# Kernel optimization log

Measured on AMD Instinct MI355X. Metric: run time of the kernel, lower is better.

The kernel has to match this reference:

```python
import jax, jax.numpy as jnp
import numpy as np

B, L, D, H, W, FF = 4, 4096, 1024, 16, 256, 4096
HD = D // H
EPS = 1e-6


def layernorm(x, gamma, beta):
    mean = x.mean(-1, keepdims=True)
    var = ((x - mean) ** 2).mean(-1, keepdims=True)  # unbiased=False
    return gamma * (x - mean) / jnp.sqrt(var + EPS) + beta


def setup_inputs() -> dict:
    key = jax.random.key(0)
    ks = jax.random.split(key, 6)
    s = 0.02
    return {
        "x": jax.random.normal(ks[0], (B, L, D), jnp.float32),
        "in_proj_w": jax.random.normal(ks[1], (3 * D, D), jnp.float32) * s,
        "in_proj_b": jnp.zeros((3 * D,), jnp.float32),
        "out_w": jax.random.normal(ks[2], (D, D), jnp.float32) * s,
        "out_b": jnp.zeros((D,), jnp.float32),
        "gamma1": jnp.ones((D,), jnp.float32),
        "beta1": jnp.zeros((D,), jnp.float32),
        "w1": jax.random.normal(ks[3], (D, FF), jnp.float32) * s,
        "bf1": jnp.zeros((FF,), jnp.float32),
        "w2": jax.random.normal(ks[4], (FF, D), jnp.float32) * s,
        "bf2": jnp.zeros((D,), jnp.float32),
        "gamma2": jnp.ones((D,), jnp.float32),
        "beta2": jnp.zeros((D,), jnp.float32),
    }


def reference(x, in_proj_w, in_proj_b, out_w, out_b, gamma1, beta1,
              w1, bf1, w2, bf2, gamma2, beta2):
    nC = L // W
    wq, wk, wv = jnp.split(in_proj_w, 3, axis=0)   # each [D, D], torch: y = x @ w.T + b
    bq, bk, bv = jnp.split(in_proj_b, 3)

    # chunk queries; kv window for chunk c = [chunk c-1, chunk c] (chunk 0: only itself)
    ch = x.reshape(B, nC, W, D)
    prev = jnp.concatenate([jnp.zeros_like(ch[:, :1]), ch[:, :-1]], axis=1)
    kv = jnp.concatenate([prev, ch], axis=2)       # [B, nC, 2W, D]

    q = (ch @ wq.T + bq).reshape(B, nC, W, H, HD)
    k = (kv @ wk.T + bk).reshape(B, nC, 2 * W, H, HD)
    v = (kv @ wv.T + bv).reshape(B, nC, 2 * W, H, HD)

    scores = jnp.einsum('bcqhd,bckhd->bchqk', q, k) / np.float32(np.sqrt(HD))
    # first W key slots of chunk 0 are padding -> mask them
    valid = (jnp.arange(2 * W)[None, :] >= W) | (jnp.arange(nC)[:, None] > 0)  # [nC, 2W]
    scores = jnp.where(valid[None, :, None, None, :], scores, jnp.float32(-1e9))
    attn = jax.nn.softmax(scores, axis=-1)

    o = jnp.einsum('bchqk,bckhd->bcqhd', attn, v).reshape(B, nC, W, D)
    attn_out = (o @ out_w.T + out_b).reshape(B, L, D)

    x1 = layernorm(x + attn_out, gamma1, beta1)
    ffn = jax.nn.relu(x1 @ w1 + bf1) @ w2 + bf2
    return layernorm(x1 + ffn, gamma2, beta2)
```

## Files before the change

kernel.cpp:

```cpp
#include <hip/hip_runtime.h>
#include <stdint.h>

#define Bsz 4
#define Lseq 4096
#define Dm 1024
#define Hh 16
#define Wc 256
#define FFd 4096
#define NC 16
#define NTOK (Bsz * Lseq)

typedef unsigned short u16;

__device__ __forceinline__ float bf2f(u16 u) {
  union { unsigned int i; float f; } v; v.i = ((unsigned int)u) << 16; return v.f;
}
__device__ __forceinline__ u16 f2bf(float f) {
  union { float f; unsigned int i; } v; v.f = f;
  unsigned int r = v.i + 0x7fffu + ((v.i >> 16) & 1u);
  return (u16)(r >> 16);
}
__device__ __forceinline__ unsigned int pack2bf(float a, float b) {
  union { float f; unsigned int u; } x, y; x.f = a; y.f = b;
  return ((x.u + 0x8000u) >> 16) | ((y.u + 0x8000u) & 0xffff0000u);
}

__global__ void cvt_f32_bf16(const float* __restrict__ in, u16* __restrict__ out, long n) {
  long i = ((long)blockIdx.x * blockDim.x + threadIdx.x) * 4;
  if (i >= n) return;
  float4 v = *(const float4*)(in + i);
  u16 o[4] = { f2bf(v.x), f2bf(v.y), f2bf(v.z), f2bf(v.w) };
  *(uint2*)(out + i) = *(const uint2*)o;
}

__global__ void transpose_f32_bf16(const float* __restrict__ in, u16* __restrict__ out,
                                   int R, int C) {
  __shared__ float tile[32][33];
  int tx = threadIdx.x & 31, ty = threadIdx.x >> 5;
  int r0 = blockIdx.y * 32, c0 = blockIdx.x * 32;
#pragma unroll
  for (int k = 0; k < 4; ++k)
    tile[ty + 8 * k][tx] = in[(size_t)(r0 + ty + 8 * k) * C + c0 + tx];
  __syncthreads();
#pragma unroll
  for (int k = 0; k < 4; ++k)
    out[(size_t)(c0 + ty + 8 * k) * R + r0 + tx] = f2bf(tile[tx][ty + 8 * k]);
}

typedef __attribute__((ext_vector_type(8))) short s16x8;
typedef __attribute__((ext_vector_type(4))) float fx4;
typedef __attribute__((address_space(1))) unsigned int as1u;
typedef __attribute__((address_space(3))) unsigned int as3u;
typedef __attribute__((address_space(3))) const u16 l16c;

__device__ __forceinline__ void gll16(const void* g, void* l) {
  __builtin_amdgcn_global_load_lds((as1u*)g, (as3u*)l, 16, 0, 0);
}

#define DSR(dst, base, IMM)                                                 \
  asm volatile("ds_read_b128 %0, %1 offset:" IMM : "=v"(dst) : "v"(base))

__device__ __forceinline__ void swizzle_mn(int MB, int NB, int* mb, int* nb) {
  int flat = blockIdx.y * NB + blockIdx.x;
  if ((MB & 7) == 0) {
    int xcd = flat & 7;
    int j = flat >> 3;
    int rpx = MB >> 3;
    *nb = j / rpx;
    int rowin = j - *nb * rpx;
    *mb = (rowin << 3) | xcd;
  } else {
    *mb = blockIdx.y; *nb = blockIdx.x;
  }
}

__device__ __forceinline__ void stage_seg(const u16* __restrict__ G, int ld, int k0,
                                          u16* L, int rb0, int rb1,
                                          int wid, int lane) {
#pragma unroll
  for (int i = 0; i < 2; ++i) {
    int j = wid * 2 + i;
    int rs = (j < 8) ? (rb0 + j * 8) : (rb1 + (j - 8) * 8);
    int grow = rs + (lane >> 3);
    int gcol = k0 + (((lane & 7) ^ (lane >> 3)) << 3);
    gll16(G + (size_t)grow * ld + gcol, L + rs * 64);
  }
}

#define MFMA_Q(MQ, NQ)                                                           \
  {                                                                              \
    _Pragma("unroll") for (int mt = 0; mt < 4; ++mt) {                           \
      _Pragma("unroll") for (int nt = 0; nt < 2; ++nt) {                         \
        acc[(MQ)*4 + mt][(NQ)*2 + nt] = __builtin_amdgcn_mfma_f32_16x16x32_bf16( \
            af[mt][0], bfr[NQ][nt][0], acc[(MQ)*4 + mt][(NQ)*2 + nt], 0, 0, 0);  \
        acc[(MQ)*4 + mt][(NQ)*2 + nt] = __builtin_amdgcn_mfma_f32_16x16x32_bf16( \
            af[mt][1], bfr[NQ][nt][1], acc[(MQ)*4 + mt][(NQ)*2 + nt], 0, 0, 0);  \
      }                                                                          \
    }                                                                            \
  }

#define WAIT_LGKM_FENCE()                                  \
  asm volatile("s_waitcnt lgkmcnt(0)" ::: "memory");       \
  __builtin_amdgcn_sched_barrier(0);

#define SB() __builtin_amdgcn_sched_barrier(0);

#define R_A_MQ0()                     \
  DSR(af[0][0], baseA0, "0");         \
  DSR(af[0][1], baseA1, "0");         \
  DSR(af[1][0], baseA0, "2048");      \
  DSR(af[1][1], baseA1, "2048");      \
  DSR(af[2][0], baseA0, "4096");      \
  DSR(af[2][1], baseA1, "4096");      \
  DSR(af[3][0], baseA0, "6144");      \
  DSR(af[3][1], baseA1, "6144");
#define R_A_MQ1()                     \
  DSR(af[0][0], baseA0, "8192");      \
  DSR(af[0][1], baseA1, "8192");      \
  DSR(af[1][0], baseA0, "10240");     \
  DSR(af[1][1], baseA1, "10240");     \
  DSR(af[2][0], baseA0, "12288");     \
  DSR(af[2][1], baseA1, "12288");     \
  DSR(af[3][0], baseA0, "14336");     \
  DSR(af[3][1], baseA1, "14336");
#define R_B_SEG0()                    \
  DSR(bfr[0][0][0], baseB0, "0");     \
  DSR(bfr[0][0][1], baseB1, "0");     \
  DSR(bfr[0][1][0], baseB0, "2048");  \
  DSR(bfr[0][1][1], baseB1, "2048");
#define R_B_SEG1()                    \
  DSR(bfr[1][0][0], baseB0, "4096");  \
  DSR(bfr[1][0][1], baseB1, "4096");  \
  DSR(bfr[1][1][0], baseB0, "6144");  \
  DSR(bfr[1][1][1], baseB1, "6144");

template <int RELU, int OUTBF16, int HASBIAS>
__global__ __launch_bounds__(512, 2) void gemm256(const u16* A, int lda,
                                                  const u16* Bm,
                                                  const float* __restrict__ bias,
                                                  void* Cp,
                                                  int M, int N, int K) {
  __shared__ __attribute__((aligned(16))) u16 As[2][256 * 64];
  __shared__ __attribute__((aligned(16))) u16 Bs[2][256 * 64];
  int tid = threadIdx.x;
  int lane = tid & 63, wid = tid >> 6;
  int lm = lane & 15, quad = lane >> 4;
  int wr = wid >> 2, wc = wid & 3;
  int mb, nb;
  swizzle_mn(gridDim.y, gridDim.x, &mb, &nb);
  int m0 = mb * 256, n0 = nb * 256;
  const u16* Ag = A + (size_t)m0 * lda;
  const u16* Bg = Bm + (size_t)n0 * K;
  int NT = K >> 6;

  int off0 = (quad ^ (lm & 7)) << 3;
  int off1 = ((4 + quad) ^ (lm & 7)) << 3;

  unsigned ldsA = (unsigned)(size_t)(l16c*)(&As[0][0]);
  unsigned ldsB = (unsigned)(size_t)(l16c*)(&Bs[0][0]);
  unsigned baseA0 = ldsA + (unsigned)(((wr * 128 + lm) * 64 + off0) * 2);
  unsigned baseA1 = ldsA + (unsigned)(((wr * 128 + lm) * 64 + off1) * 2);
  unsigned baseB0 = ldsB + (unsigned)(((wc * 64 + lm) * 64 + off0) * 2);
  unsigned baseB1 = ldsB + (unsigned)(((wc * 64 + lm) * 64 + off1) * 2);
  int sel = 32768;

  fx4 acc[8][4] = {};

  stage_seg(Ag, lda, 0, As[0], 0, 128, wid, lane);
  stage_seg(Ag, lda, 0, As[0], 64, 192, wid, lane);
  stage_seg(Bg, K, 0, Bs[0], 0, 64, wid, lane);
  stage_seg(Bg, K, 0, Bs[0], 128, 192, wid, lane);
  if (NT > 1) {
    stage_seg(Ag, lda, 64, As[1], 0, 128, wid, lane);
    stage_seg(Ag, lda, 64, As[1], 64, 192, wid, lane);
    asm volatile("s_waitcnt vmcnt(4)" ::: "memory");
  } else {
    asm volatile("s_waitcnt vmcnt(0)" ::: "memory");
  }
  __builtin_amdgcn_s_barrier();

  s16x8 af[4][2];
  s16x8 bfr[2][2][2];

  R_A_MQ0();
  R_B_SEG0();

  for (int t = 0; t < NT; ++t) {
    u16* Bn = Bs[(t + 1) & 1];
    u16* An2 = As[t & 1];
    int kn = (t + 1) << 6, kn2 = (t + 2) << 6;

    if (t + 1 < NT) stage_seg(Bg, K, kn, Bn, 0, 64, wid, lane);
    __builtin_amdgcn_s_barrier();
    WAIT_LGKM_FENCE()
    __builtin_amdgcn_s_setprio(1);
    MFMA_Q(0, 0)
    __builtin_amdgcn_s_setprio(0);
    SB()
    R_B_SEG1();
    __builtin_amdgcn_s_barrier();

    if (t + 1 < NT) stage_seg(Bg, K, kn, Bn, 128, 192, wid, lane);
    __builtin_amdgcn_s_barrier();
    WAIT_LGKM_FENCE()
    __builtin_amdgcn_s_setprio(1);
    MFMA_Q(0, 1)
    __builtin_amdgcn_s_setprio(0);
    SB()
    R_A_MQ1();
    __builtin_amdgcn_s_barrier();

    if (t + 2 < NT) stage_seg(Ag, lda, kn2, An2, 0, 128, wid, lane);
    __builtin_amdgcn_s_barrier();
    WAIT_LGKM_FENCE()
    __builtin_amdgcn_s_setprio(1);
    MFMA_Q(1, 1)
    __builtin_amdgcn_s_setprio(0);
    SB()
    __builtin_amdgcn_s_barrier();

    if (t + 2 < NT) {
      stage_seg(Ag, lda, kn2, An2, 64, 192, wid, lane);
      asm volatile("s_waitcnt vmcnt(4)" ::: "memory");
    } else if (t + 2 == NT) {
      asm volatile("s_waitcnt vmcnt(0)" ::: "memory");
    }
    __builtin_amdgcn_s_barrier();
    __builtin_amdgcn_s_setprio(1);
    MFMA_Q(1, 0)
    __builtin_amdgcn_s_setprio(0);
    SB()
    baseA0 += sel; baseA1 += sel; baseB0 += sel; baseB1 += sel; sel = -sel;
    if (t + 1 < NT) {
      R_A_MQ0();
      R_B_SEG0();
    }
    __builtin_amdgcn_s_barrier();
  }

  float* Cf = (float*)Cp;
  u16* Ch = (u16*)Cp;
#pragma unroll
  for (int ai = 0; ai < 8; ++ai) {
#pragma unroll
    for (int bi = 0; bi < 4; ++bi) {
      int col = n0 + wc * 64 + (bi >> 1) * 32 + (bi & 1) * 16 + lm;
      float bv = HASBIAS ? bias[col] : 0.f;
#pragma unroll
      for (int r = 0; r < 4; ++r) {
        int row = m0 + wr * 128 + (ai >> 2) * 64 + (ai & 3) * 16 + quad * 4 + r;
        float v = acc[ai][bi][r] + bv;
        if (RELU) v = v > 0.f ? v : 0.f;
        if (OUTBF16) Ch[(size_t)row * N + col] = f2bf(v);
        else         Cf[(size_t)row * N + col] = v;
      }
    }
  }
}

#define PADK 72
#define PADV 136
#define PADP 40
#define PADO 72

__global__ __launch_bounds__(256, 2) void attn_mfma(u16* qkv) {
  __shared__ __attribute__((aligned(16))) u16 lds[38400];
  u16* Klds  = lds;
  u16* Vtlds = lds + 9216;

  int bid = blockIdx.x;
  int h = bid & (Hh - 1);
  int c = (bid >> 4) & (NC - 1);
  int b = bid >> 8;
  int tid = threadIdx.x, lane = tid & 63, w = tid >> 6;
  int lm = lane & 15, quad = lane >> 4;
  u16* Pw = lds + 17920 + w * 5120;

  size_t rowbase = (size_t)b * Lseq;

  s16x8 qf[4][2];
#pragma unroll
  for (int nt = 0; nt < 4; ++nt)
#pragma unroll
    for (int ks = 0; ks < 2; ++ks) {
      int qtok = c * Wc + w * 64 + nt * 16 + lm;
      qf[nt][ks] = *(const s16x8*)(qkv + (rowbase + qtok) * 3072 + h * 64 + ks * 32 + quad * 8);
    }

  fx4 acc_o[4][4] = {};
  float lsum[4] = {0.f, 0.f, 0.f, 0.f};

  int nph = (c > 0) ? 4 : 2;
  int t0  = (c > 0) ? (c - 1) * Wc : 0;

  for (int ph = 0; ph < nph; ++ph) {
    int kt0 = t0 + ph * 128;
    __syncthreads();

#pragma unroll
    for (int it = 0; it < 4; ++it) {
      int s = tid + it * 256;
      int row = s >> 3, off = (s & 7) * 8;
      uint4 kv = *(const uint4*)(qkv + (rowbase + kt0 + row) * 3072 + 1024 + h * 64 + off);
      *(uint4*)(Klds + row * PADK + off) = kv;
    }
    {
      int d = lane;
      int kb = w * 32;
      u16 tmp[32];
#pragma unroll
      for (int i = 0; i < 32; ++i)
        tmp[i] = qkv[(rowbase + kt0 + kb + i) * 3072 + 2048 + h * 64 + d];
#pragma unroll
      for (int i = 0; i < 4; ++i)
        *(uint4*)(Vtlds + d * PADV + kb + i * 8) = *(const uint4*)(tmp + i * 8);
    }
    __syncthreads();

#pragma unroll
    for (int kt = 0; kt < 4; ++kt) {
      u16* Pb = Pw + (kt & 1) * 2560;
      fx4 sa[2][4] = {};
#pragma unroll
      for (int ks = 0; ks < 2; ++ks) {
        s16x8 kf0 = *(const s16x8*)(Klds + (kt * 32 + lm) * PADK + ks * 32 + quad * 8);
        s16x8 kf1 = *(const s16x8*)(Klds + (kt * 32 + 16 + lm) * PADK + ks * 32 + quad * 8);
#pragma unroll
        for (int nt = 0; nt < 4; ++nt) {
          sa[0][nt] = __builtin_amdgcn_mfma_f32_16x16x32_bf16(kf0, qf[nt][ks], sa[0][nt], 0, 0, 0);
          sa[1][nt] = __builtin_amdgcn_mfma_f32_16x16x32_bf16(kf1, qf[nt][ks], sa[1][nt], 0, 0, 0);
        }
      }
#pragma unroll
      for (int mt = 0; mt < 2; ++mt)
#pragma unroll
        for (int nt = 0; nt < 4; ++nt) {
          float e0 = __expf(sa[mt][nt][0] * 0.125f);
          float e1 = __expf(sa[mt][nt][1] * 0.125f);
          float e2 = __expf(sa[mt][nt][2] * 0.125f);
          float e3 = __expf(sa[mt][nt][3] * 0.125f);
          lsum[nt] += (e0 + e1) + (e2 + e3);
          uint2 pk; pk.x = pack2bf(e0, e1); pk.y = pack2bf(e2, e3);
          *(uint2*)(Pb + (nt * 16 + lm) * PADP + mt * 16 + quad * 4) = pk;
        }
#pragma unroll
      for (int mt = 0; mt < 4; ++mt) {
        s16x8 vf = *(const s16x8*)(Vtlds + (mt * 16 + lm) * PADV + kt * 32 + quad * 8);
#pragma unroll
        for (int nt = 0; nt < 4; ++nt) {
          s16x8 pf = *(const s16x8*)(Pb + (nt * 16 + lm) * PADP + quad * 8);
          acc_o[mt][nt] = __builtin_amdgcn_mfma_f32_16x16x32_bf16(vf, pf, acc_o[mt][nt], 0, 0, 0);
        }
      }
    }
  }

#pragma unroll
  for (int nt = 0; nt < 4; ++nt) {
    float v = lsum[nt];
    v += __shfl_xor(v, 16, 64);
    v += __shfl_xor(v, 32, 64);
    lsum[nt] = 1.f / v;
  }

  __syncthreads();
  u16* Obuf = lds;
#pragma unroll
  for (int mt = 0; mt < 4; ++mt)
#pragma unroll
    for (int nt = 0; nt < 4; ++nt) {
      float inv = lsum[nt];
      uint2 pk;
      pk.x = pack2bf(acc_o[mt][nt][0] * inv, acc_o[mt][nt][1] * inv);
      pk.y = pack2bf(acc_o[mt][nt][2] * inv, acc_o[mt][nt][3] * inv);
      int q = nt * 16 + lm;
      *(uint2*)(Obuf + (w * 64 + q) * PADO + mt * 16 + quad * 4) = pk;
    }
  __syncthreads();
#pragma unroll
  for (int it = 0; it < 8; ++it) {
    int s = tid + it * 256;
    int row = s >> 3, chunk = s & 7;
    uint4 v = *(const uint4*)(Obuf + row * PADO + chunk * 8);
    *(uint4*)(qkv + (rowbase + c * Wc + row) * 3072 + h * 64 + chunk * 8) = v;
  }
}

__device__ __forceinline__ void ln_core(float sx, float sy, float sz, float sw,
                                        const float* gamma, const float* beta, int tid,
                                        float* red, float4* outv) {
  float part = sx + sy + sz + sw;
#pragma unroll
  for (int off = 32; off > 0; off >>= 1) part += __shfl_down(part, off, 64);
  if ((tid & 63) == 0) red[tid >> 6] = part;
  __syncthreads();
  float mean = (red[0] + red[1] + red[2] + red[3]) * (1.f / 1024.f);
  __syncthreads();

  float dx = sx - mean, dy = sy - mean, dz = sz - mean, dw = sw - mean;
  float sq = dx * dx + dy * dy + dz * dz + dw * dw;
#pragma unroll
  for (int off = 32; off > 0; off >>= 1) sq += __shfl_down(sq, off, 64);
  if ((tid & 63) == 0) red[tid >> 6] = sq;
  __syncthreads();
  float var = (red[0] + red[1] + red[2] + red[3]) * (1.f / 1024.f);
  float rs = rsqrtf(var + 1e-6f);

  float4 g = *(const float4*)(gamma + tid * 4);
  float4 be = *(const float4*)(beta + tid * 4);
  outv->x = g.x * dx * rs + be.x;
  outv->y = g.y * dy * rs + be.y;
  outv->z = g.z * dz * rs + be.z;
  outv->w = g.w * dw * rs + be.w;
}

__global__ __launch_bounds__(256) void ln1_kernel(const float* __restrict__ r,
                                                  const float* __restrict__ dl,
                                                  const float* __restrict__ gamma,
                                                  const float* __restrict__ beta,
                                                  u16* __restrict__ outh) {
  __shared__ float red[4];
  int row = blockIdx.x, tid = threadIdx.x;
  size_t base = (size_t)row * Dm;
  float4 rv = *(const float4*)(r + base + tid * 4);
  float4 dv = *(const float4*)(dl + base + tid * 4);
  float4 o;
  ln_core(rv.x + dv.x, rv.y + dv.y, rv.z + dv.z, rv.w + dv.w, gamma, beta, tid, red, &o);
  u16 u[4] = { f2bf(o.x), f2bf(o.y), f2bf(o.z), f2bf(o.w) };
  *(uint2*)(outh + base + tid * 4) = *(const uint2*)u;
}

__global__ __launch_bounds__(256) void ln2_kernel(const u16* __restrict__ r,
                                                  const float* dl,
                                                  const float* __restrict__ colbias,
                                                  const float* __restrict__ gamma,
                                                  const float* __restrict__ beta,
                                                  float* outf) {
  __shared__ float red[4];
  int row = blockIdx.x, tid = threadIdx.x;
  size_t base = (size_t)row * Dm;
  uint2 ru = *(const uint2*)(r + base + tid * 4);
  const u16* pu = (const u16*)&ru;
  float4 dv = *(const float4*)(dl + base + tid * 4);
  float4 bb = *(const float4*)(colbias + tid * 4);
  float4 o;
  ln_core(bf2f(pu[0]) + dv.x + bb.x, bf2f(pu[1]) + dv.y + bb.y,
          bf2f(pu[2]) + dv.z + bb.z, bf2f(pu[3]) + dv.w + bb.w,
          gamma, beta, tid, red, &o);
  *(float4*)(outf + base + tid * 4) = o;
}

extern "C" void kernel_launch(void* const* d_in, const int* in_sizes, int n_in,
                              void* d_out, int out_size, void* d_ws, size_t ws_size,
                              hipStream_t stream) {
  const float* x         = (const float*)d_in[0];
  const float* in_proj_w = (const float*)d_in[1];
  const float* in_proj_b = (const float*)d_in[2];
  const float* out_w     = (const float*)d_in[3];
  const float* out_b     = (const float*)d_in[4];
  const float* gamma1    = (const float*)d_in[5];
  const float* beta1     = (const float*)d_in[6];
  const float* w1        = (const float*)d_in[7];
  const float* bf1       = (const float*)d_in[8];
  const float* w2        = (const float*)d_in[9];
  const float* bf2       = (const float*)d_in[10];
  const float* gamma2    = (const float*)d_in[11];
  const float* beta2     = (const float*)d_in[12];
  float* out = (float*)d_out;

  char* ws = (char*)d_ws;
  size_t off = 0;
  auto alloc = [&](size_t bytes) -> char* {
    char* p = ws + off;
    off += (bytes + 255) & ~(size_t)255;
    return p;
  };
  u16* wqkvh = (u16*)alloc((size_t)3 * Dm * Dm * 2);
  u16* owh   = (u16*)alloc((size_t)Dm * Dm * 2);
  u16* w1th  = (u16*)alloc((size_t)FFd * Dm * 2);
  u16* w2th  = (u16*)alloc((size_t)Dm * FFd * 2);
  u16* big   = (u16*)alloc((size_t)NTOK * FFd * 2);
  u16* x1h   = (u16*)alloc((size_t)NTOK * Dm * 2);
  u16* qkvh = big;
  u16* hh   = big;
  u16* xh   = (u16*)d_out;
  float* attnf = out;
  float* y2f   = out;

  cvt_f32_bf16<<<(long)NTOK * Dm / 1024, 256, 0, stream>>>(x, xh, (long)NTOK * Dm);
  cvt_f32_bf16<<<(long)3 * Dm * Dm / 1024, 256, 0, stream>>>(in_proj_w, wqkvh, (long)3 * Dm * Dm);
  cvt_f32_bf16<<<(long)Dm * Dm / 1024, 256, 0, stream>>>(out_w, owh, (long)Dm * Dm);
  transpose_f32_bf16<<<dim3(FFd / 32, Dm / 32), 256, 0, stream>>>(w1, w1th, Dm, FFd);
  transpose_f32_bf16<<<dim3(Dm / 32, FFd / 32), 256, 0, stream>>>(w2, w2th, FFd, Dm);

  gemm256<0, 1, 1><<<dim3(3 * Dm / 256, NTOK / 256), 512, 0, stream>>>(
      xh, Dm, wqkvh, in_proj_b, qkvh, NTOK, 3 * Dm, Dm);

  attn_mfma<<<Bsz * NC * Hh, 256, 0, stream>>>(qkvh);

  gemm256<0, 0, 1><<<dim3(Dm / 256, NTOK / 256), 512, 0, stream>>>(
      qkvh, 3 * Dm, owh, out_b, attnf, NTOK, Dm, Dm);

  ln1_kernel<<<NTOK, 256, 0, stream>>>(x, attnf, gamma1, beta1, x1h);

  gemm256<1, 1, 1><<<dim3(FFd / 256, NTOK / 256), 512, 0, stream>>>(
      x1h, Dm, w1th, bf1, hh, NTOK, FFd, Dm);

  gemm256<0, 0, 0><<<dim3(Dm / 256, NTOK / 256), 512, 0, stream>>>(
      hh, FFd, w2th, (const float*)nullptr, y2f, NTOK, Dm, FFd);

  ln2_kernel<<<NTOK, 256, 0, stream>>>(x1h, y2f, bf2, gamma2, beta2, out);
}
```

Baseline: 688.5 us.

## Pre-pack weights into MFMA fragment order and load B directly from global

Weights are repacked on device into an MFMA-fragment-ordered bf16 layout, so each wave can load its B operands straight from global memory into registers with dwordx4 loads, bypassing LDS. The freed LDS becomes a 4-stage ring buffer for the A tiles, and several barriers per K-step are removed. The goal is less LDS traffic and synchronisation, paid for with more global/L2 traffic on B (each wave fetches its own B fragments) and more register pressure from holding B in flight.

```diff
diff --git a/kernel.cpp b/kernel.cpp
--- a/kernel.cpp
+++ b/kernel.cpp
@@ -33,18 +33,44 @@
   *(uint2*)(out + i) = *(const uint2*)o;
 }
 
-__global__ void transpose_f32_bf16(const float* __restrict__ in, u16* __restrict__ out,
-                                   int R, int C) {
-  __shared__ float tile[32][33];
-  int tx = threadIdx.x & 31, ty = threadIdx.x >> 5;
-  int r0 = blockIdx.y * 32, c0 = blockIdx.x * 32;
-#pragma unroll
-  for (int k = 0; k < 4; ++k)
-    tile[ty + 8 * k][tx] = in[(size_t)(r0 + ty + 8 * k) * C + c0 + tx];
+
+__global__ void pack_f32_nk(const float* __restrict__ W, u16* __restrict__ P, int N, int K) {
+  long idx = (long)blockIdx.x * 256 + threadIdx.x;
+  int lane = (int)(idx & 63);
+  long c = idx >> 6;
+  int ks = (int)(c & 1);
+  long c2 = c >> 1;
+  int g = (int)(c2 % (N >> 4));
+  int t = (int)(c2 / (N >> 4));
+  int n = g * 16 + (lane & 15);
+  int k = t * 64 + ks * 32 + (lane >> 4) * 8;
+  const float* src = W + (size_t)n * K + k;
+  u16 o[8];
+#pragma unroll
+  for (int e = 0; e < 8; ++e) o[e] = f2bf(src[e]);
+  *(uint4*)(P + idx * 8) = *(const uint4*)o;
+}
+
+__global__ void transpose_pack_f32(const float* __restrict__ W, u16* __restrict__ P,
+                                   int N, int K) {
+  __shared__ float t64[64][33];
+  int tid = threadIdx.x;
+  int n0 = blockIdx.x * 32, k0 = blockIdx.y * 64;
+  int tx = tid & 31, ty = tid >> 5;
+#pragma unroll
+  for (int p = 0; p < 8; ++p)
+    t64[ty + 8 * p][tx] = W[(size_t)(k0 + ty + 8 * p) * N + n0 + tx];
   __syncthreads();
-#pragma unroll
-  for (int k = 0; k < 4; ++k)
-    out[(size_t)(c0 + ty + 8 * k) * R + r0 + tx] = f2bf(tile[tx][ty + 8 * k]);
+  int nl = tid & 31, kq = tid >> 5;
+  int ks = kq >> 2, quad = kq & 3;
+  int g = (n0 >> 4) + (nl >> 4);
+  int lmv = nl & 15;
+  int t = k0 >> 6;
+  u16 o[8];
+#pragma unroll
+  for (int e = 0; e < 8; ++e) o[e] = f2bf(t64[kq * 8 + e][nl]);
+  size_t c = ((size_t)t * (N >> 4) + g) * 2 + ks;
+  *(uint4*)(P + c * 512 + (quad * 16 + lmv) * 8) = *(const uint4*)o;
 }
 
 typedef __attribute__((ext_vector_type(8))) short s16x8;
@@ -59,6 +85,9 @@
 
 #define DSR(dst, base, IMM)                                                 \
   asm volatile("ds_read_b128 %0, %1 offset:" IMM : "=v"(dst) : "v"(base))
+
+#define GLB(dst, addr, IMM)                                                 \
+  asm volatile("global_load_dwordx4 %0, %1, off offset:" IMM : "=v"(dst) : "v"(addr))
 
 __device__ __forceinline__ void swizzle_mn(int MB, int NB, int* mb, int* nb) {
   int flat = blockIdx.y * NB + blockIdx.x;
@@ -123,25 +152,23 @@
   DSR(af[2][1], baseA1, "12288");     \
   DSR(af[3][0], baseA0, "14336");     \
   DSR(af[3][1], baseA1, "14336");
-#define R_B_SEG0()                    \
-  DSR(bfr[0][0][0], baseB0, "0");     \
-  DSR(bfr[0][0][1], baseB1, "0");     \
-  DSR(bfr[0][1][0], baseB0, "2048");  \
-  DSR(bfr[0][1][1], baseB1, "2048");
-#define R_B_SEG1()                    \
-  DSR(bfr[1][0][0], baseB0, "4096");  \
-  DSR(bfr[1][0][1], baseB1, "4096");  \
-  DSR(bfr[1][1][0], baseB0, "6144");  \
-  DSR(bfr[1][1][1], baseB1, "6144");
+#define R_B_ALL()                        \
+  GLB(bfr[0][0][0], bq0, "0");           \
+  GLB(bfr[0][0][1], bq0, "1024");        \
+  GLB(bfr[0][1][0], bq1, "0");           \
+  GLB(bfr[0][1][1], bq1, "1024");        \
+  GLB(bfr[1][0][0], bq2, "0");           \
+  GLB(bfr[1][0][1], bq2, "1024");        \
+  GLB(bfr[1][1][0], bq3, "0");           \
+  GLB(bfr[1][1][1], bq3, "1024");
 
 template <int RELU, int OUTBF16, int HASBIAS>
-__global__ __launch_bounds__(512, 2) void gemm256(const u16* A, int lda,
-                                                  const u16* Bm,
-                                                  const float* __restrict__ bias,
-                                                  void* Cp,
-                                                  int M, int N, int K) {
-  __shared__ __attribute__((aligned(16))) u16 As[2][256 * 64];
-  __shared__ __attribute__((aligned(16))) u16 Bs[2][256 * 64];
+__global__ __launch_bounds__(512, 2) void gemm256p(const u16* A, int lda,
+                                                   const u16* Bp,
+                                                   const float* __restrict__ bias,
+                                                   void* Cp,
+                                                   int M, int N, int K) {
+  __shared__ __attribute__((aligned(16))) u16 As[4][256 * 64];
   int tid = threadIdx.x;
   int lane = tid & 63, wid = tid >> 6;
   int lm = lane & 15, quad = lane >> 4;
@@ -150,90 +177,74 @@
   swizzle_mn(gridDim.y, gridDim.x, &mb, &nb);
   int m0 = mb * 256, n0 = nb * 256;
   const u16* Ag = A + (size_t)m0 * lda;
-  const u16* Bg = Bm + (size_t)n0 * K;
   int NT = K >> 6;
 
   int off0 = (quad ^ (lm & 7)) << 3;
   int off1 = ((4 + quad) ^ (lm & 7)) << 3;
-
   unsigned ldsA = (unsigned)(size_t)(l16c*)(&As[0][0]);
-  unsigned ldsB = (unsigned)(size_t)(l16c*)(&Bs[0][0]);
-  unsigned baseA0 = ldsA + (unsigned)(((wr * 128 + lm) * 64 + off0) * 2);
-  unsigned baseA1 = ldsA + (unsigned)(((wr * 128 + lm) * 64 + off1) * 2);
-  unsigned baseB0 = ldsB + (unsigned)(((wc * 64 + lm) * 64 + off0) * 2);
-  unsigned baseB1 = ldsB + (unsigned)(((wc * 64 + lm) * 64 + off1) * 2);
-  int sel = 32768;
+  unsigned rootA0 = ldsA + (unsigned)(((wr * 128 + lm) * 64 + off0) * 2);
+  unsigned rootA1 = ldsA + (unsigned)(((wr * 128 + lm) * 64 + off1) * 2);
+
+  size_t bstep = (size_t)(N >> 4) * 1024;
+  const u16* bq0 = Bp + (size_t)(nb * 16 + wc * 4 + 0) * 1024 + lane * 8;
+  const u16* bq1 = bq0 + 1024;
+  const u16* bq2 = bq0 + 2048;
+  const u16* bq3 = bq0 + 3072;
 
   fx4 acc[8][4] = {};
+  s16x8 af[4][2];
+  s16x8 bfr[2][2][2];
 
   stage_seg(Ag, lda, 0, As[0], 0, 128, wid, lane);
   stage_seg(Ag, lda, 0, As[0], 64, 192, wid, lane);
-  stage_seg(Bg, K, 0, Bs[0], 0, 64, wid, lane);
-  stage_seg(Bg, K, 0, Bs[0], 128, 192, wid, lane);
   if (NT > 1) {
     stage_seg(Ag, lda, 64, As[1], 0, 128, wid, lane);
     stage_seg(Ag, lda, 64, As[1], 64, 192, wid, lane);
-    asm volatile("s_waitcnt vmcnt(4)" ::: "memory");
-  } else {
-    asm volatile("s_waitcnt vmcnt(0)" ::: "memory");
-  }
+  }
+  if (NT > 2) {
+    stage_seg(Ag, lda, 128, As[2], 0, 128, wid, lane);
+    stage_seg(Ag, lda, 128, As[2], 64, 192, wid, lane);
+  }
+  R_B_ALL();
+  asm volatile("s_waitcnt vmcnt(8)" ::: "memory");
   __builtin_amdgcn_s_barrier();
 
-  s16x8 af[4][2];
-  s16x8 bfr[2][2][2];
-
-  R_A_MQ0();
-  R_B_SEG0();
-
-  for (int t = 0; t < NT; ++t) {
-    u16* Bn = Bs[(t + 1) & 1];
-    u16* An2 = As[t & 1];
-    int kn = (t + 1) << 6, kn2 = (t + 2) << 6;
-
-    if (t + 1 < NT) stage_seg(Bg, K, kn, Bn, 0, 64, wid, lane);
-    __builtin_amdgcn_s_barrier();
+  for (int s = 0; s < NT; ++s) {
+    unsigned bsel = (unsigned)((s & 3) << 15);
+    unsigned baseA0 = rootA0 + bsel, baseA1 = rootA1 + bsel;
+    int k3 = (s + 3) << 6;
+    u16* An3 = As[(s + 3) & 3];
+    SB()
+    R_A_MQ0();
+    if (s + 3 < NT) {
+      stage_seg(Ag, lda, k3, An3, 0, 128, wid, lane);
+      asm volatile("s_waitcnt vmcnt(2)" ::: "memory");
+    } else {
+      asm volatile("s_waitcnt vmcnt(0)" ::: "memory");
+    }
     WAIT_LGKM_FENCE()
     __builtin_amdgcn_s_setprio(1);
     MFMA_Q(0, 0)
     __builtin_amdgcn_s_setprio(0);
     SB()
-    R_B_SEG1();
-    __builtin_amdgcn_s_barrier();
-
-    if (t + 1 < NT) stage_seg(Bg, K, kn, Bn, 128, 192, wid, lane);
-    __builtin_amdgcn_s_barrier();
-    WAIT_LGKM_FENCE()
+    if (s + 3 < NT) stage_seg(Ag, lda, k3, An3, 64, 192, wid, lane);
     __builtin_amdgcn_s_setprio(1);
     MFMA_Q(0, 1)
     __builtin_amdgcn_s_setprio(0);
     SB()
     R_A_MQ1();
-    __builtin_amdgcn_s_barrier();
-
-    if (t + 2 < NT) stage_seg(Ag, lda, kn2, An2, 0, 128, wid, lane);
-    __builtin_amdgcn_s_barrier();
     WAIT_LGKM_FENCE()
     __builtin_amdgcn_s_setprio(1);
     MFMA_Q(1, 1)
     __builtin_amdgcn_s_setprio(0);
     SB()
-    __builtin_amdgcn_s_barrier();
-
-    if (t + 2 < NT) {
-      stage_seg(Ag, lda, kn2, An2, 64, 192, wid, lane);
-      asm volatile("s_waitcnt vmcnt(4)" ::: "memory");
-    } else if (t + 2 == NT) {
-      asm volatile("s_waitcnt vmcnt(0)" ::: "memory");
-    }
-    __builtin_amdgcn_s_barrier();
     __builtin_amdgcn_s_setprio(1);
     MFMA_Q(1, 0)
     __builtin_amdgcn_s_setprio(0);
     SB()
-    baseA0 += sel; baseA1 += sel; baseB0 += sel; baseB1 += sel; sel = -sel;
-    if (t + 1 < NT) {
-      R_A_MQ0();
-      R_B_SEG0();
+    if (s + 1 < NT) {
+      bq0 += bstep; bq1 += bstep; bq2 += bstep; bq3 += bstep;
+      R_B_ALL();
     }
     __builtin_amdgcn_s_barrier();
   }
@@ -475,10 +486,10 @@
     off += (bytes + 255) & ~(size_t)255;
     return p;
   };
-  u16* wqkvh = (u16*)alloc((size_t)3 * Dm * Dm * 2);
-  u16* owh   = (u16*)alloc((size_t)Dm * Dm * 2);
-  u16* w1th  = (u16*)alloc((size_t)FFd * Dm * 2);
-  u16* w2th  = (u16*)alloc((size_t)Dm * FFd * 2);
+  u16* wqkvp = (u16*)alloc((size_t)3 * Dm * Dm * 2);
+  u16* owp   = (u16*)alloc((size_t)Dm * Dm * 2);
+  u16* w1p   = (u16*)alloc((size_t)FFd * Dm * 2);
+  u16* w2p   = (u16*)alloc((size_t)Dm * FFd * 2);
   u16* big   = (u16*)alloc((size_t)NTOK * FFd * 2);
   u16* x1h   = (u16*)alloc((size_t)NTOK * Dm * 2);
   u16* qkvh = big;
@@ -488,26 +499,26 @@
   float* y2f   = out;
 
   cvt_f32_bf16<<<(long)NTOK * Dm / 1024, 256, 0, stream>>>(x, xh, (long)NTOK * Dm);
-  cvt_f32_bf16<<<(long)3 * Dm * Dm / 1024, 256, 0, stream>>>(in_proj_w, wqkvh, (long)3 * Dm * Dm);
-  cvt_f32_bf16<<<(long)Dm * Dm / 1024, 256, 0, stream>>>(out_w, owh, (long)Dm * Dm);
-  transpose_f32_bf16<<<dim3(FFd / 32, Dm / 32), 256, 0, stream>>>(w1, w1th, Dm, FFd);
-  transpose_f32_bf16<<<dim3(Dm / 32, FFd / 32), 256, 0, stream>>>(w2, w2th, FFd, Dm);
-
-  gemm256<0, 1, 1><<<dim3(3 * Dm / 256, NTOK / 256), 512, 0, stream>>>(
-      xh, Dm, wqkvh, in_proj_b, qkvh, NTOK, 3 * Dm, Dm);
+  pack_f32_nk<<<(3 * Dm * Dm) / 2048, 256, 0, stream>>>(in_proj_w, wqkvp, 3 * Dm, Dm);
+  pack_f32_nk<<<(Dm * Dm) / 2048, 256, 0, stream>>>(out_w, owp, Dm, Dm);
+  transpose_pack_f32<<<dim3(FFd / 32, Dm / 64), 256, 0, stream>>>(w1, w1p, FFd, Dm);
+  transpose_pack_f32<<<dim3(Dm / 32, FFd / 64), 256, 0, stream>>>(w2, w2p, Dm, FFd);
+
+  gemm256p<0, 1, 1><<<dim3(3 * Dm / 256, NTOK / 256), 512, 0, stream>>>(
+      xh, Dm, wqkvp, in_proj_b, qkvh, NTOK, 3 * Dm, Dm);
 
   attn_mfma<<<Bsz * NC * Hh, 256, 0, stream>>>(qkvh);
 
-  gemm256<0, 0, 1><<<dim3(Dm / 256, NTOK / 256), 512, 0, stream>>>(
-      qkvh, 3 * Dm, owh, out_b, attnf, NTOK, Dm, Dm);
+  gemm256p<0, 0, 1><<<dim3(Dm / 256, NTOK / 256), 512, 0, stream>>>(
+      qkvh, 3 * Dm, owp, out_b, attnf, NTOK, Dm, Dm);
 
   ln1_kernel<<<NTOK, 256, 0, stream>>>(x, attnf, gamma1, beta1, x1h);
 
-  gemm256<1, 1, 1><<<dim3(FFd / 256, NTOK / 256), 512, 0, stream>>>(
-      x1h, Dm, w1th, bf1, hh, NTOK, FFd, Dm);
-
-  gemm256<0, 0, 0><<<dim3(Dm / 256, NTOK / 256), 512, 0, stream>>>(
-      hh, FFd, w2th, (const float*)nullptr, y2f, NTOK, Dm, FFd);
+  gemm256p<1, 1, 1><<<dim3(FFd / 256, NTOK / 256), 512, 0, stream>>>(
+      x1h, Dm, w1p, bf1, hh, NTOK, FFd, Dm);
+
+  gemm256p<0, 0, 0><<<dim3(Dm / 256, NTOK / 256), 512, 0, stream>>>(
+      hh, FFd, w2p, (const float*)nullptr, y2f, NTOK, Dm, FFd);
 
   ln2_kernel<<<NTOK, 256, 0, stream>>>(x1h, y2f, bf2, gamma2, beta2, out);
 }
```

Result: no change. 679.1 us (-1.4%).

## Restructure GEMM main loop into eight-phase pipeline with precomputed load pointers

Applied to the files above, without the earlier changes.

Rewrites the bf16 GEMM k-loop so each 64-wide step issues LDS fragment reads at the start of each phase, interleaved with global-to-LDS loads split into quarter-tile segments. Global and LDS addresses are computed once before the loop and advanced incrementally, and the per-step stage_seg helper and its index arithmetic are removed. The prologue now stages two A tiles plus B ahead, and vmcnt and lgkmcnt waits are retuned. The aim is better overlap of global loads, LDS reads and MFMA work, at the cost of subtler buffer-hazard ordering between the two LDS buffers.

```diff
diff --git a/kernel.cpp b/kernel.cpp
--- a/kernel.cpp
+++ b/kernel.cpp
@@ -74,19 +74,6 @@
   }
 }
 
-__device__ __forceinline__ void stage_seg(const u16* __restrict__ G, int ld, int k0,
-                                          u16* L, int rb0, int rb1,
-                                          int wid, int lane) {
-#pragma unroll
-  for (int i = 0; i < 2; ++i) {
-    int j = wid * 2 + i;
-    int rs = (j < 8) ? (rb0 + j * 8) : (rb1 + (j - 8) * 8);
-    int grow = rs + (lane >> 3);
-    int gcol = k0 + (((lane & 7) ^ (lane >> 3)) << 3);
-    gll16(G + (size_t)grow * ld + gcol, L + rs * 64);
-  }
-}
-
 #define MFMA_Q(MQ, NQ)                                                           \
   {                                                                              \
     _Pragma("unroll") for (int mt = 0; mt < 4; ++mt) {                           \
@@ -103,43 +90,41 @@
   asm volatile("s_waitcnt lgkmcnt(0)" ::: "memory");       \
   __builtin_amdgcn_sched_barrier(0);
 
-#define SB() __builtin_amdgcn_sched_barrier(0);
-
 #define R_A_MQ0()                     \
-  DSR(af[0][0], baseA0, "0");         \
-  DSR(af[0][1], baseA1, "0");         \
-  DSR(af[1][0], baseA0, "2048");      \
-  DSR(af[1][1], baseA1, "2048");      \
-  DSR(af[2][0], baseA0, "4096");      \
-  DSR(af[2][1], baseA1, "4096");      \
-  DSR(af[3][0], baseA0, "6144");      \
-  DSR(af[3][1], baseA1, "6144");
+  DSR(af[0][0], bA0, "0");            \
+  DSR(af[0][1], bA1, "0");            \
+  DSR(af[1][0], bA0, "2048");         \
+  DSR(af[1][1], bA1, "2048");         \
+  DSR(af[2][0], bA0, "4096");         \
+  DSR(af[2][1], bA1, "4096");         \
+  DSR(af[3][0], bA0, "6144");         \
+  DSR(af[3][1], bA1, "6144");
 #define R_A_MQ1()                     \
-  DSR(af[0][0], baseA0, "8192");      \
-  DSR(af[0][1], baseA1, "8192");      \
-  DSR(af[1][0], baseA0, "10240");     \
-  DSR(af[1][1], baseA1, "10240");     \
-  DSR(af[2][0], baseA0, "12288");     \
-  DSR(af[2][1], baseA1, "12288");     \
-  DSR(af[3][0], baseA0, "14336");     \
-  DSR(af[3][1], baseA1, "14336");
-#define R_B_SEG0()                    \
-  DSR(bfr[0][0][0], baseB0, "0");     \
-  DSR(bfr[0][0][1], baseB1, "0");     \
-  DSR(bfr[0][1][0], baseB0, "2048");  \
-  DSR(bfr[0][1][1], baseB1, "2048");
-#define R_B_SEG1()                    \
-  DSR(bfr[1][0][0], baseB0, "4096");  \
-  DSR(bfr[1][0][1], baseB1, "4096");  \
-  DSR(bfr[1][1][0], baseB0, "6144");  \
-  DSR(bfr[1][1][1], baseB1, "6144");
+  DSR(af[0][0], bA0, "8192");         \
+  DSR(af[0][1], bA1, "8192");         \
+  DSR(af[1][0], bA0, "10240");        \
+  DSR(af[1][1], bA1, "10240");        \
+  DSR(af[2][0], bA0, "12288");        \
+  DSR(af[2][1], bA1, "12288");        \
+  DSR(af[3][0], bA0, "14336");        \
+  DSR(af[3][1], bA1, "14336");
+#define R_B_NQ0()                     \
+  DSR(bfr[0][0][0], bB0, "0");        \
+  DSR(bfr[0][0][1], bB1, "0");        \
+  DSR(bfr[0][1][0], bB0, "2048");     \
+  DSR(bfr[0][1][1], bB1, "2048");
+#define R_B_NQ1()                     \
+  DSR(bfr[1][0][0], bB0, "4096");     \
+  DSR(bfr[1][0][1], bB1, "4096");     \
+  DSR(bfr[1][1][0], bB0, "6144");     \
+  DSR(bfr[1][1][1], bB1, "6144");
 
 template <int RELU, int OUTBF16, int HASBIAS>
-__global__ __launch_bounds__(512, 2) void gemm256(const u16* A, int lda,
-                                                  const u16* Bm,
-                                                  const float* __restrict__ bias,
-                                                  void* Cp,
-                                                  int M, int N, int K) {
+__global__ __launch_bounds__(512, 2) void gemm8p(const u16* A, int lda,
+                                                 const u16* Bm,
+                                                 const float* __restrict__ bias,
+                                                 void* Cp,
+                                                 int M, int N, int K) {
   __shared__ __attribute__((aligned(16))) u16 As[2][256 * 64];
   __shared__ __attribute__((aligned(16))) u16 Bs[2][256 * 64];
   int tid = threadIdx.x;
@@ -155,87 +140,105 @@
 
   int off0 = (quad ^ (lm & 7)) << 3;
   int off1 = ((4 + quad) ^ (lm & 7)) << 3;
-
   unsigned ldsA = (unsigned)(size_t)(l16c*)(&As[0][0]);
   unsigned ldsB = (unsigned)(size_t)(l16c*)(&Bs[0][0]);
   unsigned baseA0 = ldsA + (unsigned)(((wr * 128 + lm) * 64 + off0) * 2);
   unsigned baseA1 = ldsA + (unsigned)(((wr * 128 + lm) * 64 + off1) * 2);
   unsigned baseB0 = ldsB + (unsigned)(((wc * 64 + lm) * 64 + off0) * 2);
   unsigned baseB1 = ldsB + (unsigned)(((wc * 64 + lm) * 64 + off1) * 2);
-  int sel = 32768;
+
+  int j0 = wid * 2, j1 = wid * 2 + 1;
+  int rA0a = (j0 < 8) ? j0 * 8 : 128 + (j0 - 8) * 8;
+  int rA0b = (j1 < 8) ? j1 * 8 : 128 + (j1 - 8) * 8;
+  int rA1a = rA0a + 64, rA1b = rA0b + 64;
+  int rB0a = (j0 >> 2) * 64 + (j0 & 3) * 8;
+  int rB0b = (j1 >> 2) * 64 + (j1 & 3) * 8;
+  int rB1a = rB0a + 32, rB1b = rB0b + 32;
+  int lrow = lane >> 3;
+  int gsw = ((lane & 7) ^ lrow) << 3;
+  const u16* pA0a = Ag + (size_t)(rA0a + lrow) * lda + gsw;
+  const u16* pA0b = Ag + (size_t)(rA0b + lrow) * lda + gsw;
+  const u16* pA1a = Ag + (size_t)(rA1a + lrow) * lda + gsw;
+  const u16* pA1b = Ag + (size_t)(rA1b + lrow) * lda + gsw;
+  const u16* pB0a = Bg + (size_t)(rB0a + lrow) * K + gsw;
+  const u16* pB0b = Bg + (size_t)(rB0b + lrow) * K + gsw;
+  const u16* pB1a = Bg + (size_t)(rB1a + lrow) * K + gsw;
+  const u16* pB1b = Bg + (size_t)(rB1b + lrow) * K + gsw;
+  char* AsB = (char*)&As[0][0];
+  char* BsB = (char*)&Bs[0][0];
+  unsigned dA0a = (unsigned)rA0a * 128, dA0b = (unsigned)rA0b * 128;
+  unsigned dA1a = (unsigned)rA1a * 128, dA1b = (unsigned)rA1b * 128;
+  unsigned dB0a = (unsigned)rB0a * 128, dB0b = (unsigned)rB0b * 128;
+  unsigned dB1a = (unsigned)rB1a * 128, dB1b = (unsigned)rB1b * 128;
 
   fx4 acc[8][4] = {};
-
-  stage_seg(Ag, lda, 0, As[0], 0, 128, wid, lane);
-  stage_seg(Ag, lda, 0, As[0], 64, 192, wid, lane);
-  stage_seg(Bg, K, 0, Bs[0], 0, 64, wid, lane);
-  stage_seg(Bg, K, 0, Bs[0], 128, 192, wid, lane);
-  if (NT > 1) {
-    stage_seg(Ag, lda, 64, As[1], 0, 128, wid, lane);
-    stage_seg(Ag, lda, 64, As[1], 64, 192, wid, lane);
-    asm volatile("s_waitcnt vmcnt(4)" ::: "memory");
-  } else {
-    asm volatile("s_waitcnt vmcnt(0)" ::: "memory");
-  }
-  __builtin_amdgcn_s_barrier();
-
   s16x8 af[4][2];
   s16x8 bfr[2][2][2];
 
-  R_A_MQ0();
-  R_B_SEG0();
-
-  for (int t = 0; t < NT; ++t) {
-    u16* Bn = Bs[(t + 1) & 1];
-    u16* An2 = As[t & 1];
-    int kn = (t + 1) << 6, kn2 = (t + 2) << 6;
-
-    if (t + 1 < NT) stage_seg(Bg, K, kn, Bn, 0, 64, wid, lane);
+  gll16(pA0a, AsB + dA0a);  gll16(pA0b, AsB + dA0b);
+  gll16(pB0a, BsB + dB0a);  gll16(pB0b, BsB + dB0b);
+  gll16(pB1a, BsB + dB1a);  gll16(pB1b, BsB + dB1b);
+  gll16(pA1a, AsB + dA1a);  gll16(pA1b, AsB + dA1b);
+  gll16(pA0a + 64, AsB + 32768 + dA0a);  gll16(pA0b + 64, AsB + 32768 + dA0b);
+  gll16(pB0a + 64, BsB + 32768 + dB0a);  gll16(pB0b + 64, BsB + 32768 + dB0b);
+  gll16(pA1a + 64, AsB + 32768 + dA1a);  gll16(pA1b + 64, AsB + 32768 + dA1b);
+  pA0a += 128; pA0b += 128; pA1a += 128; pA1b += 128;
+  pB0a += 128; pB0b += 128;
+  pB1a += 64;  pB1b += 64;
+  asm volatile("s_waitcnt vmcnt(6)" ::: "memory");
+  __builtin_amdgcn_s_barrier();
+
+  for (int s = 0; s < NT; ++s) {
+    unsigned bsel = (unsigned)((s & 1) << 15);
+    unsigned bA0 = baseA0 + bsel, bA1 = baseA1 + bsel;
+    unsigned bB0 = baseB0 + bsel, bB1 = baseB1 + bsel;
+    char* bufA = AsB + bsel;
+    char* bufB = BsB + bsel;
+    char* bufBn = BsB + (bsel ^ 32768);
+
+    R_A_MQ0();
+    R_B_NQ0();
+    if (s + 1 < NT) { gll16(pB1a, bufBn + dB1a); gll16(pB1b, bufBn + dB1b); }
+    asm volatile("s_waitcnt lgkmcnt(8)" ::: "memory");
     __builtin_amdgcn_s_barrier();
     WAIT_LGKM_FENCE()
     __builtin_amdgcn_s_setprio(1);
     MFMA_Q(0, 0)
     __builtin_amdgcn_s_setprio(0);
-    SB()
-    R_B_SEG1();
-    __builtin_amdgcn_s_barrier();
-
-    if (t + 1 < NT) stage_seg(Bg, K, kn, Bn, 128, 192, wid, lane);
+    __builtin_amdgcn_s_barrier();
+
+    R_B_NQ1();
+    if (s + 2 < NT) { gll16(pA0a, bufA + dA0a); gll16(pA0b, bufA + dA0b); }
     __builtin_amdgcn_s_barrier();
     WAIT_LGKM_FENCE()
     __builtin_amdgcn_s_setprio(1);
     MFMA_Q(0, 1)
     __builtin_amdgcn_s_setprio(0);
-    SB()
+    __builtin_amdgcn_s_barrier();
+
     R_A_MQ1();
-    __builtin_amdgcn_s_barrier();
-
-    if (t + 2 < NT) stage_seg(Ag, lda, kn2, An2, 0, 128, wid, lane);
+    if (s + 2 < NT) { gll16(pB0a, bufB + dB0a); gll16(pB0b, bufB + dB0b); }
     __builtin_amdgcn_s_barrier();
     WAIT_LGKM_FENCE()
     __builtin_amdgcn_s_setprio(1);
     MFMA_Q(1, 1)
     __builtin_amdgcn_s_setprio(0);
-    SB()
-    __builtin_amdgcn_s_barrier();
-
-    if (t + 2 < NT) {
-      stage_seg(Ag, lda, kn2, An2, 64, 192, wid, lane);
-      asm volatile("s_waitcnt vmcnt(4)" ::: "memory");
-    } else if (t + 2 == NT) {
+    __builtin_amdgcn_s_barrier();
+
+    if (s + 2 < NT) {
+      gll16(pA1a, bufA + dA1a); gll16(pA1b, bufA + dA1b);
+      asm volatile("s_waitcnt vmcnt(6)" ::: "memory");
+    } else {
       asm volatile("s_waitcnt vmcnt(0)" ::: "memory");
     }
     __builtin_amdgcn_s_barrier();
     __builtin_amdgcn_s_setprio(1);
     MFMA_Q(1, 0)
     __builtin_amdgcn_s_setprio(0);
-    SB()
-    baseA0 += sel; baseA1 += sel; baseB0 += sel; baseB1 += sel; sel = -sel;
-    if (t + 1 < NT) {
-      R_A_MQ0();
-      R_B_SEG0();
-    }
-    __builtin_amdgcn_s_barrier();
+    __builtin_amdgcn_s_barrier();
+
+    pA0a += 64; pA0b += 64; pA1a += 64; pA1b += 64;
+    pB0a += 64; pB0b += 64; pB1a += 64; pB1b += 64;
   }
 
   float* Cf = (float*)Cp;
@@ -493,20 +496,20 @@
   transpose_f32_bf16<<<dim3(FFd / 32, Dm / 32), 256, 0, stream>>>(w1, w1th, Dm, FFd);
   transpose_f32_bf16<<<dim3(Dm / 32, FFd / 32), 256, 0, stream>>>(w2, w2th, FFd, Dm);
 
-  gemm256<0, 1, 1><<<dim3(3 * Dm / 256, NTOK / 256), 512, 0, stream>>>(
+  gemm8p<0, 1, 1><<<dim3(3 * Dm / 256, NTOK / 256), 512, 0, stream>>>(
       xh, Dm, wqkvh, in_proj_b, qkvh, NTOK, 3 * Dm, Dm);
 
   attn_mfma<<<Bsz * NC * Hh, 256, 0, stream>>>(qkvh);
 
-  gemm256<0, 0, 1><<<dim3(Dm / 256, NTOK / 256), 512, 0, stream>>>(
+  gemm8p<0, 0, 1><<<dim3(Dm / 256, NTOK / 256), 512, 0, stream>>>(
       qkvh, 3 * Dm, owh, out_b, attnf, NTOK, Dm, Dm);
 
   ln1_kernel<<<NTOK, 256, 0, stream>>>(x, attnf, gamma1, beta1, x1h);
 
-  gemm256<1, 1, 1><<<dim3(FFd / 256, NTOK / 256), 512, 0, stream>>>(
+  gemm8p<1, 1, 1><<<dim3(FFd / 256, NTOK / 256), 512, 0, stream>>>(
       x1h, Dm, w1th, bf1, hh, NTOK, FFd, Dm);
 
-  gemm256<0, 0, 0><<<dim3(Dm / 256, NTOK / 256), 512, 0, stream>>>(
+  gemm8p<0, 0, 0><<<dim3(Dm / 256, NTOK / 256), 512, 0, stream>>>(
       hh, FFd, w2th, (const float*)nullptr, y2f, NTOK, Dm, FFd);
 
   ln2_kernel<<<NTOK, 256, 0, stream>>>(x1h, y2f, bf2, gamma2, beta2, out);
```

After: 682.1 us. Within noise of the previous version (-0.9%).
